# Optimization experiments

Measured on AMD Instinct MI355X. Metric: run time of the kernel, lower is better.

The kernel has to match this reference:

```python
import jax, jax.numpy as jnp
import numpy as np

S, B, T, I, H, O = 8, 32, 512, 256, 512, 32


def setup_inputs() -> dict:
    key = jax.random.key(0)
    ks = jax.random.split(key, 8)
    x = jax.random.normal(ks[0], (S, B, T, I), dtype=jnp.float32)
    lengths = jax.random.randint(ks[1], (S,), T // 2, T + 1, dtype=jnp.int32)
    s = 1.0 / np.sqrt(H)
    u = lambda k, shp: jax.random.uniform(k, shp, jnp.float32, -s, s)
    return {
        'x': x,
        'lengths': lengths,
        'W_ih': u(ks[2], (3 * H, I)),
        'W_hh': u(ks[3], (3 * H, H)),
        'b_ih': u(ks[4], (3 * H,)),
        'b_hh': u(ks[5], (3 * H,)),
        'W_out': u(ks[6], (O, H)),
        'b_out': u(ks[7], (O,)),
    }


def reference(x, lengths, W_ih, W_hh, b_ih, b_hh, W_out, b_out):
    # x: [S, B, T, I] padded ragged batch; lengths: [S] valid steps per sequence.
    # Precompute input projections for all gates in one big GEMM: [S, B, T, 3H]
    xW = jnp.einsum('sbti,gi->sbtg', x, W_ih) + b_ih

    def run_seq(xw, length):
        # xw: [B, T, 3H]; one ragged 'sequence' (a mini-batch in the original list)
        def step(h, inp):
            xw_t, t = inp  # xw_t: [B, 3H]
            hW = h @ W_hh.T + b_hh
            xr, xz, xn = jnp.split(xw_t, 3, axis=-1)
            hr, hz, hn = jnp.split(hW, 3, axis=-1)
            r = jax.nn.sigmoid(xr + hr)
            z = jax.nn.sigmoid(xz + hz)
            n = jnp.tanh(xn + r * hn)
            h_new = (1.0 - z) * n + z * h
            # freeze hidden state past the valid length -> h ends at step length-1
            h = jnp.where(t < length, h_new, h)
            return h, None

        h0 = jnp.zeros((B, H), dtype=xw.dtype)
        hT, _ = jax.lax.scan(step, h0, (jnp.swapaxes(xw, 0, 1), jnp.arange(T)))
        return hT.mean(axis=0)  # output[:, -1].mean(0) -> [H]

    hbar = jax.vmap(run_seq)(xW, lengths)  # [S, H]
    return hbar @ W_out.T + b_out  # [S, O]
```

## Files before the change

### kernel.cpp

```cpp
#include <hip/hip_runtime.h>
#include <hip/hip_bf16.h>

#define S_ 8
#define B_ 32
#define T_ 512
#define I_ 256
#define H_ 512
#define O_ 32

typedef __attribute__((ext_vector_type(8))) short short8;
typedef __attribute__((ext_vector_type(4))) float float4_;

__device__ inline unsigned short f2bf(float f) {
    unsigned u = __float_as_uint(f);
    u = (u + 0x7fffu + ((u >> 16) & 1u)) >> 16;
    return (unsigned short)u;
}

__device__ inline short8 load_cvt8(const float* p) {
    float4_ a = *reinterpret_cast<const float4_*>(p);
    float4_ b = *reinterpret_cast<const float4_*>(p + 4);
    short8 r;
    r[0] = (short)f2bf(a[0]); r[1] = (short)f2bf(a[1]);
    r[2] = (short)f2bf(a[2]); r[3] = (short)f2bf(a[3]);
    r[4] = (short)f2bf(b[0]); r[5] = (short)f2bf(b[1]);
    r[6] = (short)f2bf(b[2]); r[7] = (short)f2bf(b[3]);
    return r;
}

__device__ inline short8 load_h16_coherent(const unsigned short* p) {
    short8 v;
    asm volatile("global_load_dwordx4 %0, %1, off sc0 sc1"
                 : "=v"(v) : "v"(p) : "memory");
    return v;
}
__device__ inline void store_h2_coherent(unsigned short* p, unsigned v) {
    asm volatile("global_store_short %0, %1, off sc0 sc1"
                 :: "v"(p), "v"(v) : "memory");
}
__device__ inline void wait_vm0_fence() {
    asm volatile("s_waitcnt vmcnt(0)" ::: "memory");
    __builtin_amdgcn_sched_barrier(0);
}

#define WS_NEED 544768

__global__ __launch_bounds__(256, 1)
void zgru_persistent(const float* __restrict__ x, const int* __restrict__ lens,
                     const float* __restrict__ Wih, const float* __restrict__ Whh,
                     const float* __restrict__ bih, const float* __restrict__ bhh,
                     const float* __restrict__ Wout, const float* __restrict__ bout,
                     float* __restrict__ out,
                     unsigned short* __restrict__ hbuf, float* __restrict__ hbar,
                     unsigned* __restrict__ step_ctr, unsigned* __restrict__ done_ctr)
{
    const int tid  = threadIdx.x;
    const int wg   = blockIdx.x;
    const int s    = wg >> 5;
    const int j    = wg & 31;
    const int wid  = tid >> 6;
    const int lane = tid & 63;
    const int m    = wid >> 1;
    const int kh   = wid & 1;
    const int lrow = lane & 15;
    const int lgrp = lane >> 4;

    const int len = lens[s];

    short8 bhR[8], bhZ[8], bhN[8];
    short8 bxR[4], bxZ[4], bxN[4];
    {
        const int gr = 16 * j + lrow;
        #pragma unroll
        for (int kc = 0; kc < 8; ++kc) {
            const int k0 = 256 * kh + 32 * kc + 8 * lgrp;
            bhR[kc] = load_cvt8(Whh + (size_t)(gr          ) * H_ + k0);
            bhZ[kc] = load_cvt8(Whh + (size_t)(gr +     H_ ) * H_ + k0);
            bhN[kc] = load_cvt8(Whh + (size_t)(gr + 2 * H_ ) * H_ + k0);
        }
        #pragma unroll
        for (int kc = 0; kc < 4; ++kc) {
            const int k0 = 128 * kh + 32 * kc + 8 * lgrp;
            bxR[kc] = load_cvt8(Wih + (size_t)(gr          ) * I_ + k0);
            bxZ[kc] = load_cvt8(Wih + (size_t)(gr +     H_ ) * I_ + k0);
            bxN[kc] = load_cvt8(Wih + (size_t)(gr + 2 * H_ ) * I_ + k0);
        }
        #pragma unroll
        for (int kc = 0; kc < 8; ++kc)
            asm volatile("" : "+v"(bhR[kc]), "+v"(bhZ[kc]), "+v"(bhN[kc]));
        #pragma unroll
        for (int kc = 0; kc < 4; ++kc)
            asm volatile("" : "+v"(bxR[kc]), "+v"(bxZ[kc]), "+v"(bxN[kc]));
    }

    const int gcol   = 16 * j + lrow;
    const float bsR  = bih[gcol] + bhh[gcol];
    const float bsZ  = bih[H_ + gcol] + bhh[H_ + gcol];
    const float biN  = bih[2 * H_ + gcol];
    const float bhN_ = bhh[2 * H_ + gcol];

    float h[4] = {0.f, 0.f, 0.f, 0.f};

    __shared__ float4_ xch[2][4][64];
    __shared__ unsigned last_flag;
    __shared__ float red[8][32];

    const size_t HBUF = (size_t)S_ * B_ * H_;
    const int arow = 16 * m + lrow;

    for (int t = 0; t < len; ++t) {
        float4_ aR = {0,0,0,0}, aZ = {0,0,0,0}, aNX = {0,0,0,0};
        {
            const float* xb = x + (((size_t)s * B_ + arow) * T_ + t) * I_ + 128 * kh + 8 * lgrp;
            #pragma unroll
            for (int kc = 0; kc < 4; ++kc) {
                short8 ax = load_cvt8(xb + 32 * kc);
                aR  = __builtin_amdgcn_mfma_f32_16x16x32_bf16(ax, bxR[kc], aR, 0, 0, 0);
                aZ  = __builtin_amdgcn_mfma_f32_16x16x32_bf16(ax, bxZ[kc], aZ, 0, 0, 0);
                aNX = __builtin_amdgcn_mfma_f32_16x16x32_bf16(ax, bxN[kc], aNX, 0, 0, 0);
            }
        }

        if (t > 0) {
            __syncthreads();
            if (tid == 0) {
                __hip_atomic_fetch_add(&step_ctr[s * 64], 1u, __ATOMIC_RELAXED, __HIP_MEMORY_SCOPE_AGENT);
                const unsigned tgt = 32u * (unsigned)t;
                while (__hip_atomic_load(&step_ctr[s * 64], __ATOMIC_RELAXED, __HIP_MEMORY_SCOPE_AGENT) < tgt)
                    __builtin_amdgcn_s_sleep(1);
            }
            __syncthreads();
        }

        const unsigned short* hr = hbuf + (size_t)(t & 1) * HBUF + (size_t)s * B_ * H_;
        short8 ah[8];
        #pragma unroll
        for (int kc = 0; kc < 8; ++kc) {
            const int k0 = 256 * kh + 32 * kc + 8 * lgrp;
            ah[kc] = load_h16_coherent(hr + (size_t)arow * H_ + k0);
        }
        wait_vm0_fence();

        float4_ aNH = {0,0,0,0};
        #pragma unroll
        for (int kc = 0; kc < 8; ++kc) {
            aR  = __builtin_amdgcn_mfma_f32_16x16x32_bf16(ah[kc], bhR[kc], aR, 0, 0, 0);
            aZ  = __builtin_amdgcn_mfma_f32_16x16x32_bf16(ah[kc], bhZ[kc], aZ, 0, 0, 0);
            aNH = __builtin_amdgcn_mfma_f32_16x16x32_bf16(ah[kc], bhN[kc], aNH, 0, 0, 0);
        }

        if (kh == 1) {
            xch[m][0][lane] = aR;
            xch[m][1][lane] = aZ;
            xch[m][2][lane] = aNH;
            xch[m][3][lane] = aNX;
        }
        __syncthreads();
        if (kh == 0) {
            aR  += xch[m][0][lane];
            aZ  += xch[m][1][lane];
            aNH += xch[m][2][lane];
            aNX += xch[m][3][lane];
            unsigned short* hw = hbuf + (size_t)((t + 1) & 1) * HBUF + (size_t)s * B_ * H_;
            #pragma unroll
            for (int i = 0; i < 4; ++i) {
                const float pr = aR[i] + bsR;
                const float pz = aZ[i] + bsZ;
                const float r = 1.f / (1.f + __expf(-pr));
                const float z = 1.f / (1.f + __expf(-pz));
                const float pn = aNX[i] + biN + r * (aNH[i] + bhN_);
                const float e = __expf(-2.f * fabsf(pn));
                float n = (1.f - e) / (1.f + e);
                n = copysignf(n, pn);
                h[i] = z * (h[i] - n) + n;
                store_h2_coherent(hw + (size_t)(16 * m + 4 * lgrp + i) * H_ + gcol,
                                  (unsigned)f2bf(h[i]));
            }
        }
        __syncthreads();
    }

    float s4 = h[0] + h[1] + h[2] + h[3];
    s4 += __shfl_xor(s4, 16);
    s4 += __shfl_xor(s4, 32);
    if (kh == 0 && lgrp == 0)
        atomicAdd(&hbar[(size_t)s * H_ + gcol], s4);

    __syncthreads();
    if (tid == 0) {
        unsigned old = __hip_atomic_fetch_add(&done_ctr[s * 64], 1u, __ATOMIC_RELAXED, __HIP_MEMORY_SCOPE_AGENT);
        last_flag = (old == 31u) ? 1u : 0u;
    }
    __syncthreads();
    if (last_flag) {
        const int o = tid & 31;
        const int p = tid >> 5;
        float acc = 0.f;
        const float* hb = hbar + (size_t)s * H_;
        const float* wr = Wout + (size_t)o * H_;
        for (int hh = 64 * p; hh < 64 * p + 64; ++hh) {
            float hv = __hip_atomic_load(&hb[hh], __ATOMIC_RELAXED, __HIP_MEMORY_SCOPE_AGENT);
            acc += hv * wr[hh];
        }
        red[p][o] = acc;
        __syncthreads();
        if (tid < 32) {
            float v = 0.f;
            #pragma unroll
            for (int q = 0; q < 8; ++q) v += red[q][tid];
            out[s * O_ + tid] = v * (1.f / 32.f) + bout[tid];
        }
    }
}

extern "C" void kernel_launch(void* const* d_in, const int* in_sizes, int n_in,
                              void* d_out, int out_size, void* d_ws, size_t ws_size,
                              hipStream_t stream) {
    (void)in_sizes; (void)n_in; (void)out_size; (void)ws_size;
    const float* x    = (const float*)d_in[0];
    const int*   lens = (const int*)d_in[1];
    const float* Wih  = (const float*)d_in[2];
    const float* Whh  = (const float*)d_in[3];
    const float* bih  = (const float*)d_in[4];
    const float* bhh  = (const float*)d_in[5];
    const float* Wout = (const float*)d_in[6];
    const float* bout = (const float*)d_in[7];
    float* out = (float*)d_out;

    char* wsc = (char*)d_ws;
    unsigned short* hbuf = (unsigned short*)wsc;
    float*    hbar = (float*)(wsc + 524288);
    unsigned* sctr = (unsigned*)(wsc + 540672);
    unsigned* dctr = (unsigned*)(wsc + 542720);

    hipMemsetAsync(d_ws, 0, WS_NEED, stream);

    zgru_persistent<<<dim3(256), dim3(256), 0, stream>>>(
        x, lens, Wih, Whh, bih, bhh, Wout, bout, out, hbuf, hbar, sctr, dctr);
}
```

Baseline: 2.136 ms.

## Replace atomic step counter barrier with per-wave flag polling and double-buffered LDS

Swaps the per-step group barrier (one atomic add plus a single-thread spin, wrapped in two __syncthreads) for per-wave progress flags. Each finishing wave writes its step number, and every wave polls all 64 flags of its sequence with a coherent load and a ballot. The trailing __syncthreads is removed by double-buffering the LDS exchange buffer. Block-to-sequence mapping is also interleaved (s = wg & 7) to spread each sequence's workgroups across the device. The intent is lower latency on the serial recurrence path, at the cost of more polling traffic and a subtle memory-ordering dependency on the waitcnt before each flag store.

```diff
diff --git a/kernel.cpp b/kernel.cpp
--- a/kernel.cpp
+++ b/kernel.cpp
@@ -34,8 +34,18 @@
                  : "=v"(v) : "v"(p) : "memory");
     return v;
 }
+__device__ inline unsigned load_u32_coherent(const unsigned* p) {
+    unsigned v;
+    asm volatile("global_load_dword %0, %1, off sc0 sc1"
+                 : "=v"(v) : "v"(p) : "memory");
+    return v;
+}
 __device__ inline void store_h2_coherent(unsigned short* p, unsigned v) {
     asm volatile("global_store_short %0, %1, off sc0 sc1"
+                 :: "v"(p), "v"(v) : "memory");
+}
+__device__ inline void store_u32_coherent(unsigned* p, unsigned v) {
+    asm volatile("global_store_dword %0, %1, off sc0 sc1"
                  :: "v"(p), "v"(v) : "memory");
 }
 __device__ inline void wait_vm0_fence() {
@@ -52,12 +62,12 @@
                      const float* __restrict__ Wout, const float* __restrict__ bout,
                      float* __restrict__ out,
                      unsigned short* __restrict__ hbuf, float* __restrict__ hbar,
-                     unsigned* __restrict__ step_ctr, unsigned* __restrict__ done_ctr)
+                     unsigned* __restrict__ flags, unsigned* __restrict__ done_ctr)
 {
     const int tid  = threadIdx.x;
     const int wg   = blockIdx.x;
-    const int s    = wg >> 5;
-    const int j    = wg & 31;
+    const int s    = wg & 7;
+    const int j    = wg >> 3;
     const int wid  = tid >> 6;
     const int lane = tid & 63;
     const int m    = wid >> 1;
@@ -101,12 +111,14 @@
 
     float h[4] = {0.f, 0.f, 0.f, 0.f};
 
-    __shared__ float4_ xch[2][4][64];
+    __shared__ float4_ xch[2][2][4][64];
     __shared__ unsigned last_flag;
     __shared__ float red[8][32];
 
     const size_t HBUF = (size_t)S_ * B_ * H_;
     const int arow = 16 * m + lrow;
+    const unsigned* fl = flags + s * 64;
+    unsigned* myflag = flags + s * 64 + j * 2 + m;
 
     for (int t = 0; t < len; ++t) {
         float4_ aR = {0,0,0,0}, aZ = {0,0,0,0}, aNX = {0,0,0,0};
@@ -122,14 +134,13 @@
         }
 
         if (t > 0) {
-            __syncthreads();
-            if (tid == 0) {
-                __hip_atomic_fetch_add(&step_ctr[s * 64], 1u, __ATOMIC_RELAXED, __HIP_MEMORY_SCOPE_AGENT);
-                const unsigned tgt = 32u * (unsigned)t;
-                while (__hip_atomic_load(&step_ctr[s * 64], __ATOMIC_RELAXED, __HIP_MEMORY_SCOPE_AGENT) < tgt)
-                    __builtin_amdgcn_s_sleep(1);
+            const unsigned tgt = (unsigned)t;
+            for (;;) {
+                unsigned fv = load_u32_coherent(fl + lane);
+                asm volatile("s_waitcnt vmcnt(0)" ::: "memory");
+                if (__ballot(fv >= tgt) == ~0ull) break;
             }
-            __syncthreads();
+            __builtin_amdgcn_sched_barrier(0);
         }
 
         const unsigned short* hr = hbuf + (size_t)(t & 1) * HBUF + (size_t)s * B_ * H_;
@@ -150,17 +161,17 @@
         }
 
         if (kh == 1) {
-            xch[m][0][lane] = aR;
-            xch[m][1][lane] = aZ;
-            xch[m][2][lane] = aNH;
-            xch[m][3][lane] = aNX;
+            xch[t & 1][m][0][lane] = aR;
+            xch[t & 1][m][1][lane] = aZ;
+            xch[t & 1][m][2][lane] = aNH;
+            xch[t & 1][m][3][lane] = aNX;
         }
         __syncthreads();
         if (kh == 0) {
-            aR  += xch[m][0][lane];
-            aZ  += xch[m][1][lane];
-            aNH += xch[m][2][lane];
-            aNX += xch[m][3][lane];
+            aR  += xch[t & 1][m][0][lane];
+            aZ  += xch[t & 1][m][1][lane];
+            aNH += xch[t & 1][m][2][lane];
+            aNX += xch[t & 1][m][3][lane];
             unsigned short* hw = hbuf + (size_t)((t + 1) & 1) * HBUF + (size_t)s * B_ * H_;
             #pragma unroll
             for (int i = 0; i < 4; ++i) {
@@ -176,8 +187,10 @@
                 store_h2_coherent(hw + (size_t)(16 * m + 4 * lgrp + i) * H_ + gcol,
                                   (unsigned)f2bf(h[i]));
             }
-        }
-        __syncthreads();
+            asm volatile("s_waitcnt vmcnt(0)" ::: "memory");
+            if (lane == 0)
+                store_u32_coherent(myflag, (unsigned)(t + 1));
+        }
     }
 
     float s4 = h[0] + h[1] + h[2] + h[3];
@@ -229,12 +242,12 @@
 
     char* wsc = (char*)d_ws;
     unsigned short* hbuf = (unsigned short*)wsc;
-    float*    hbar = (float*)(wsc + 524288);
-    unsigned* sctr = (unsigned*)(wsc + 540672);
-    unsigned* dctr = (unsigned*)(wsc + 542720);
+    float*    hbar  = (float*)(wsc + 524288);
+    unsigned* flags = (unsigned*)(wsc + 540672);
+    unsigned* dctr  = (unsigned*)(wsc + 542720);
 
     hipMemsetAsync(d_ws, 0, WS_NEED, stream);
 
     zgru_persistent<<<dim3(256), dim3(256), 0, stream>>>(
-        x, lens, Wih, Whh, bih, bhh, Wout, bout, out, hbuf, hbar, sctr, dctr);
-}
+        x, lens, Wih, Whh, bih, bhh, Wout, bout, out, hbuf, hbar, flags, dctr);
+}
```

Result: slower. 2.474 ms (+15.9%).
